# Performance work log

Measured on AMD Instinct MI355X. Metric: run time of the kernel, lower is better.

## Reference

```python
import jax, jax.numpy as jnp
import numpy as np

HIDDEN = 1024
INTER = 4096
EPS = 1e-12


def _ste(q, x):
    # straight-through estimator: forward q, backward identity wrt x
    return x + jax.lax.stop_gradient(q - x)


def setup_inputs() -> dict:
    key = jax.random.key(0)
    ks = jax.random.split(key, 4)
    hidden_states = jax.random.normal(ks[0], (4, 2048, INTER), dtype=jnp.float32)
    input_tensor = jax.random.normal(ks[1], (4, 2048, HIDDEN), dtype=jnp.float32)
    W = jax.random.normal(ks[2], (HIDDEN, INTER), dtype=jnp.float32) * 0.02
    b = jnp.zeros((HIDDEN,), dtype=jnp.float32)
    clip_val = jnp.asarray(2.5, dtype=jnp.float32)  # learnable elastic alpha
    gamma = jnp.ones((HIDDEN,), dtype=jnp.float32)
    beta = jnp.zeros((HIDDEN,), dtype=jnp.float32)
    return {"hidden_states": hidden_states, "input_tensor": input_tensor,
            "W": W, "b": b, "clip_val": clip_val, "gamma": gamma, "beta": beta}


def reference(hidden_states, input_tensor, W, b, clip_val, gamma, beta):
    # --- binary weight (BWN): per-output-channel scale = mean(|W|, axis=in) ---
    w_scale = jnp.mean(jnp.abs(W), axis=1, keepdims=True)  # [hidden, 1]
    W_q = _ste(w_scale * jnp.sign(W), W)                    # [hidden, inter]
    # --- elastic signed binary activation: q = alpha * sign(x / alpha) ---
    s = hidden_states / clip_val
    x_q = clip_val * _ste(jnp.sign(s), s)                   # [b, s, inter]
    # --- dense projection ---
    h = jnp.einsum('bsi,hi->bsh', x_q, W_q) + b             # [b, s, hidden]
    # dropout prob 0.0 (eval mode) -> no-op
    # --- residual + LayerNorm (eps=1e-12) ---
    r = h + input_tensor
    mu = jnp.mean(r, axis=-1, keepdims=True)
    var = jnp.mean(jnp.square(r - mu), axis=-1, keepdims=True)
    out = (r - mu) * jax.lax.rsqrt(var + EPS) * gamma + beta
    return out
```

## Files before the change

kernel.cpp:

```cpp
#include <hip/hip_runtime.h>
#include <stdint.h>

#define HIDDEN 1024
#define INTER  4096
#define ROWS   8192
#define BM     128
#define BN     128
#define NKSTEP 64
#define NBLK   512
#define BSTEP  65536

typedef int i32x4 __attribute__((ext_vector_type(4)));

__device__ __forceinline__ uint32_t sgn4(float4 v) {
    uint32_t b0 = (v.x < 0.f) ? 0xFFu : 0x01u;
    uint32_t b1 = (v.y < 0.f) ? 0xFFu : 0x01u;
    uint32_t b2 = (v.z < 0.f) ? 0xFFu : 0x01u;
    uint32_t b3 = (v.w < 0.f) ? 0xFFu : 0x01u;
    return b0 | (b1 << 8) | (b2 << 16) | (b3 << 24);
}

__global__ __launch_bounds__(256)
void pack_w_kernel(const float* __restrict__ W, uint8_t* __restrict__ Bg,
                   float* __restrict__ wscale) {
    int h = blockIdx.x;
    int tid = threadIdx.x;
    int lane = tid & 63, wv = tid >> 6;
    const float4* row = (const float4*)(W + (size_t)h * INTER);
    const uint32_t base_h = (uint32_t)(h >> 4) * 1024u + (uint32_t)(h & 15) * 16u;
    float asum = 0.f;
    #pragma unroll
    for (int q = 0; q < 4; ++q) {
        int g = q * 256 + tid;
        float4 v = row[g];
        asum += fabsf(v.x) + fabsf(v.y) + fabsf(v.z) + fabsf(v.w);
        uint32_t off = (uint32_t)(g >> 4) * (uint32_t)BSTEP + base_h
                     + (uint32_t)((g & 15) >> 2) * 256u + (uint32_t)(g & 3) * 4u;
        *(uint32_t*)(Bg + off) = sgn4(v);
    }
    #pragma unroll
    for (int off = 32; off > 0; off >>= 1) asum += __shfl_down(asum, off);
    __shared__ float red[4];
    if (lane == 0) red[wv] = asum;
    __syncthreads();
    if (tid == 0) wscale[h] = (red[0] + red[1] + red[2] + red[3]) * (1.0f / INTER);
}

__global__ __launch_bounds__(512, 4)
void gemm_kernel(const float* __restrict__ hs, const float* __restrict__ input,
                 const float* __restrict__ bias, const float* __restrict__ clipp,
                 float* __restrict__ out, const uint8_t* __restrict__ Bg,
                 const float* __restrict__ wscale) {
    __shared__ alignas(16) uint8_t sA[2 * 8192];

    const int tid  = threadIdx.x;
    const int lane = tid & 63;
    const int wave = tid >> 6;
    const int mt   = blockIdx.x & 63;
    const int ch   = blockIdx.x >> 6;
    const int m0   = mt * BM;

    const int r  = tid >> 2;
    const int kc = tid & 3;
    const int awofs = (r >> 4) * 1024 + (kc * 16 + (r & 15)) * 16;
    const float* aload = hs + (size_t)(m0 + r) * INTER + kc * 16;

    const uint8_t* bbase = Bg + (size_t)(ch * 8 + wave) * 1024 + lane * 16;
    const int fofs = lane * 16;

    i32x4 acc[8];
    #pragma unroll
    for (int rt = 0; rt < 8; ++rt) acc[rt] = (i32x4){0, 0, 0, 0};
    i32x4 Bb0, Bb1;
    float4 av0, av1, av2, av3;

    av0 = *(const float4*)(aload + 0);
    av1 = *(const float4*)(aload + 4);
    av2 = *(const float4*)(aload + 8);
    av3 = *(const float4*)(aload + 12);
    Bb0 = *(const i32x4*)(bbase);
    {
        i32x4 sg = (i32x4){(int)sgn4(av0), (int)sgn4(av1),
                           (int)sgn4(av2), (int)sgn4(av3)};
        *(i32x4*)&sA[awofs] = sg;
    }
    av0 = *(const float4*)(aload + 64);
    av1 = *(const float4*)(aload + 68);
    av2 = *(const float4*)(aload + 72);
    av3 = *(const float4*)(aload + 76);
    asm volatile("s_waitcnt lgkmcnt(0)" ::: "memory");
    __builtin_amdgcn_s_barrier();

#define BODY(T, CUR, BC, BN_, PFB, PFA) do {                                   \
    const uint8_t* ab_ = sA + (CUR) * 8192;                                    \
    i32x4 af0_ = *(const i32x4*)&ab_[0 * 1024 + fofs];                         \
    i32x4 af1_ = *(const i32x4*)&ab_[1 * 1024 + fofs];                         \
    i32x4 af2_ = *(const i32x4*)&ab_[2 * 1024 + fofs];                         \
    i32x4 af3_ = *(const i32x4*)&ab_[3 * 1024 + fofs];                         \
    i32x4 af4_ = *(const i32x4*)&ab_[4 * 1024 + fofs];                         \
    i32x4 af5_ = *(const i32x4*)&ab_[5 * 1024 + fofs];                         \
    i32x4 af6_ = *(const i32x4*)&ab_[6 * 1024 + fofs];                         \
    i32x4 af7_ = *(const i32x4*)&ab_[7 * 1024 + fofs];                         \
    if (PFB) Bb##BN_ = *(const i32x4*)(bbase + (size_t)((T) + 1) * BSTEP);     \
    __builtin_amdgcn_s_setprio(1);                                             \
    acc[0] = __builtin_amdgcn_mfma_i32_16x16x64_i8(af0_, Bb##BC, acc[0], 0, 0, 0); \
    acc[1] = __builtin_amdgcn_mfma_i32_16x16x64_i8(af1_, Bb##BC, acc[1], 0, 0, 0); \
    acc[2] = __builtin_amdgcn_mfma_i32_16x16x64_i8(af2_, Bb##BC, acc[2], 0, 0, 0); \
    acc[3] = __builtin_amdgcn_mfma_i32_16x16x64_i8(af3_, Bb##BC, acc[3], 0, 0, 0); \
    acc[4] = __builtin_amdgcn_mfma_i32_16x16x64_i8(af4_, Bb##BC, acc[4], 0, 0, 0); \
    acc[5] = __builtin_amdgcn_mfma_i32_16x16x64_i8(af5_, Bb##BC, acc[5], 0, 0, 0); \
    acc[6] = __builtin_amdgcn_mfma_i32_16x16x64_i8(af6_, Bb##BC, acc[6], 0, 0, 0); \
    acc[7] = __builtin_amdgcn_mfma_i32_16x16x64_i8(af7_, Bb##BC, acc[7], 0, 0, 0); \
    __builtin_amdgcn_s_setprio(0);                                             \
    if (PFB) {                                                                 \
        i32x4 sg_ = (i32x4){(int)sgn4(av0), (int)sgn4(av1),                    \
                            (int)sgn4(av2), (int)sgn4(av3)};                   \
        *(i32x4*)&sA[((CUR) ^ 1) * 8192 + awofs] = sg_;                        \
        if (PFA) {                                                             \
            av0 = *(const float4*)(aload + ((T) + 2) * 64 + 0);                \
            av1 = *(const float4*)(aload + ((T) + 2) * 64 + 4);                \
            av2 = *(const float4*)(aload + ((T) + 2) * 64 + 8);                \
            av3 = *(const float4*)(aload + ((T) + 2) * 64 + 12);               \
        }                                                                      \
        asm volatile("s_waitcnt lgkmcnt(0)" ::: "memory");                     \
        __builtin_amdgcn_s_barrier();                                          \
    }                                                                          \
} while (0)

    for (int tt = 0; tt < 31; ++tt) {
        BODY(2 * tt,     0, 0, 1, 1, 1);
        BODY(2 * tt + 1, 1, 1, 0, 1, 1);
    }
    BODY(62, 0, 0, 1, 1, 0);
    BODY(63, 1, 1, 0, 0, 0);
#undef BODY

    const float clip = clipp[0];
    const int l15 = lane & 15;
    const int gcol = ch * BN + wave * 16 + l15;
    const float cw = clip * wscale[gcol];
    const float bi = bias[gcol];
    const int rbase = (lane >> 4) * 4;
    #pragma unroll
    for (int rt = 0; rt < 8; ++rt) {
        #pragma unroll
        for (int rg = 0; rg < 4; ++rg) {
            size_t gidx = (size_t)(m0 + rt * 16 + rbase + rg) * HIDDEN + gcol;
            out[gidx] = fmaf((float)acc[rt][rg], cw, bi + input[gidx]);
        }
    }
}

__global__ __launch_bounds__(256)
void ln_kernel(float* __restrict__ out, const float* __restrict__ gamma,
               const float* __restrict__ beta) {
    const int lane = threadIdx.x & 63;
    const int wave = threadIdx.x >> 6;
    const int row  = blockIdx.x * 4 + wave;
    float4* rowp = (float4*)(out + (size_t)row * HIDDEN);
    const float4* gm4 = (const float4*)gamma;
    const float4* bt4 = (const float4*)beta;

    float4 v0 = rowp[lane +   0];
    float4 v1 = rowp[lane +  64];
    float4 v2 = rowp[lane + 128];
    float4 v3 = rowp[lane + 192];
    float s = v0.x + v0.y + v0.z + v0.w + v1.x + v1.y + v1.z + v1.w
            + v2.x + v2.y + v2.z + v2.w + v3.x + v3.y + v3.z + v3.w;
    float q = v0.x * v0.x + v0.y * v0.y + v0.z * v0.z + v0.w * v0.w
            + v1.x * v1.x + v1.y * v1.y + v1.z * v1.z + v1.w * v1.w
            + v2.x * v2.x + v2.y * v2.y + v2.z * v2.z + v2.w * v2.w
            + v3.x * v3.x + v3.y * v3.y + v3.z * v3.z + v3.w * v3.w;
    #pragma unroll
    for (int off = 1; off < 64; off <<= 1) {
        s += __shfl_xor(s, off);
        q += __shfl_xor(q, off);
    }
    float mu  = s * (1.0f / HIDDEN);
    float var = fmaf(-mu, mu, q * (1.0f / HIDDEN));
    float rs  = rsqrtf(var + 1e-12f);

    #pragma unroll
    for (int j = 0; j < 4; ++j) {
        int idx = lane + j * 64;
        float4 y = (j == 0) ? v0 : (j == 1) ? v1 : (j == 2) ? v2 : v3;
        float4 g = gm4[idx], b = bt4[idx];
        float4 o;
        o.x = (y.x - mu) * rs * g.x + b.x;
        o.y = (y.y - mu) * rs * g.y + b.y;
        o.z = (y.z - mu) * rs * g.z + b.z;
        o.w = (y.w - mu) * rs * g.w + b.w;
        rowp[idx] = o;
    }
}

extern "C" void kernel_launch(void* const* d_in, const int* in_sizes, int n_in,
                              void* d_out, int out_size, void* d_ws, size_t ws_size,
                              hipStream_t stream) {
    const float* hs    = (const float*)d_in[0];
    const float* inp   = (const float*)d_in[1];
    const float* W     = (const float*)d_in[2];
    const float* b     = (const float*)d_in[3];
    const float* clip  = (const float*)d_in[4];
    const float* gamma = (const float*)d_in[5];
    const float* beta  = (const float*)d_in[6];
    float* out = (float*)d_out;

    uint8_t* Bg   = (uint8_t*)d_ws;
    float* wscale = (float*)((char*)d_ws + 4u * 1024u * 1024u);

    pack_w_kernel<<<HIDDEN, 256, 0, stream>>>(W, Bg, wscale);
    gemm_kernel<<<NBLK, 512, 0, stream>>>(hs, inp, b, clip, out, Bg, wscale);
    ln_kernel<<<ROWS / 4, 256, 0, stream>>>(out, gamma, beta);
}
```

Before: 314.4 us.

## Pre-pack activation signs to int8 and use register-tiled GEMM without LDS

Adds a separate kernel that converts hidden_states to packed int8 signs in an MFMA-friendly layout in the workspace. The GEMM now loads both A and B fragments directly from global memory into registers, using a 2x2 wave grid with 4x4 MFMA tiles per wave, with no shared memory or barriers. Previously each 128x128 block re-read fp32 activations for every column chunk and converted them in-kernel. The change reduces fp32 traffic inside the GEMM but adds an extra pass that writes and reads 32 MB of int8 A, and relies on L2 for reuse of A across the 8 column tiles.

```diff
diff --git a/kernel.cpp b/kernel.cpp
--- a/kernel.cpp
+++ b/kernel.cpp
@@ -4,11 +4,9 @@
 #define HIDDEN 1024
 #define INTER  4096
 #define ROWS   8192
-#define BM     128
-#define BN     128
 #define NKSTEP 64
-#define NBLK   512
-#define BSTEP  65536
+#define B_KSTEP 65536
+#define A_KSTEP 524288
 
 typedef int i32x4 __attribute__((ext_vector_type(4)));
 
@@ -19,6 +17,7 @@
     uint32_t b3 = (v.w < 0.f) ? 0xFFu : 0x01u;
     return b0 | (b1 << 8) | (b2 << 16) | (b3 << 24);
 }
+
 
 __global__ __launch_bounds__(256)
 void pack_w_kernel(const float* __restrict__ W, uint8_t* __restrict__ Bg,
@@ -34,7 +33,7 @@
         int g = q * 256 + tid;
         float4 v = row[g];
         asum += fabsf(v.x) + fabsf(v.y) + fabsf(v.z) + fabsf(v.w);
-        uint32_t off = (uint32_t)(g >> 4) * (uint32_t)BSTEP + base_h
+        uint32_t off = (uint32_t)(g >> 4) * (uint32_t)B_KSTEP + base_h
                      + (uint32_t)((g & 15) >> 2) * 256u + (uint32_t)(g & 3) * 4u;
         *(uint32_t*)(Bg + off) = sgn4(v);
     }
@@ -46,107 +45,101 @@
     if (tid == 0) wscale[h] = (red[0] + red[1] + red[2] + red[3]) * (1.0f / INTER);
 }
 
-__global__ __launch_bounds__(512, 4)
-void gemm_kernel(const float* __restrict__ hs, const float* __restrict__ input,
-                 const float* __restrict__ bias, const float* __restrict__ clipp,
-                 float* __restrict__ out, const uint8_t* __restrict__ Bg,
+__global__ __launch_bounds__(256)
+void pack_a_kernel(const float* __restrict__ hs, uint8_t* __restrict__ Ag) {
+    int m = blockIdx.x;
+    int tid = threadIdx.x;
+    const float4* row = (const float4*)(hs + (size_t)m * INTER);
+    const uint32_t base_m = (uint32_t)(m >> 4) * 1024u + (uint32_t)(m & 15) * 16u;
+    #pragma unroll
+    for (int q = 0; q < 4; ++q) {
+        int g = q * 256 + tid;
+        float4 v = row[g];
+        uint32_t off = (uint32_t)(g >> 4) * (uint32_t)A_KSTEP + base_m
+                     + (uint32_t)((g & 15) >> 2) * 256u + (uint32_t)(g & 3) * 4u;
+        *(uint32_t*)(Ag + off) = sgn4(v);
+    }
+}
+
+__global__ __launch_bounds__(256, 3)
+void gemm_kernel(const float* __restrict__ input, const float* __restrict__ bias,
+                 const float* __restrict__ clipp, float* __restrict__ out,
+                 const uint8_t* __restrict__ Ag, const uint8_t* __restrict__ Bg,
                  const float* __restrict__ wscale) {
-    __shared__ alignas(16) uint8_t sA[2 * 8192];
-
     const int tid  = threadIdx.x;
     const int lane = tid & 63;
     const int wave = tid >> 6;
-    const int mt   = blockIdx.x & 63;
-    const int ch   = blockIdx.x >> 6;
-    const int m0   = mt * BM;
-
-    const int r  = tid >> 2;
-    const int kc = tid & 3;
-    const int awofs = (r >> 4) * 1024 + (kc * 16 + (r & 15)) * 16;
-    const float* aload = hs + (size_t)(m0 + r) * INTER + kc * 16;
-
-    const uint8_t* bbase = Bg + (size_t)(ch * 8 + wave) * 1024 + lane * 16;
-    const int fofs = lane * 16;
-
-    i32x4 acc[8];
-    #pragma unroll
-    for (int rt = 0; rt < 8; ++rt) acc[rt] = (i32x4){0, 0, 0, 0};
-    i32x4 Bb0, Bb1;
-    float4 av0, av1, av2, av3;
-
-    av0 = *(const float4*)(aload + 0);
-    av1 = *(const float4*)(aload + 4);
-    av2 = *(const float4*)(aload + 8);
-    av3 = *(const float4*)(aload + 12);
-    Bb0 = *(const i32x4*)(bbase);
-    {
-        i32x4 sg = (i32x4){(int)sgn4(av0), (int)sgn4(av1),
-                           (int)sgn4(av2), (int)sgn4(av3)};
-        *(i32x4*)&sA[awofs] = sg;
-    }
-    av0 = *(const float4*)(aload + 64);
-    av1 = *(const float4*)(aload + 68);
-    av2 = *(const float4*)(aload + 72);
-    av3 = *(const float4*)(aload + 76);
-    asm volatile("s_waitcnt lgkmcnt(0)" ::: "memory");
-    __builtin_amdgcn_s_barrier();
-
-#define BODY(T, CUR, BC, BN_, PFB, PFA) do {                                   \
-    const uint8_t* ab_ = sA + (CUR) * 8192;                                    \
-    i32x4 af0_ = *(const i32x4*)&ab_[0 * 1024 + fofs];                         \
-    i32x4 af1_ = *(const i32x4*)&ab_[1 * 1024 + fofs];                         \
-    i32x4 af2_ = *(const i32x4*)&ab_[2 * 1024 + fofs];                         \
-    i32x4 af3_ = *(const i32x4*)&ab_[3 * 1024 + fofs];                         \
-    i32x4 af4_ = *(const i32x4*)&ab_[4 * 1024 + fofs];                         \
-    i32x4 af5_ = *(const i32x4*)&ab_[5 * 1024 + fofs];                         \
-    i32x4 af6_ = *(const i32x4*)&ab_[6 * 1024 + fofs];                         \
-    i32x4 af7_ = *(const i32x4*)&ab_[7 * 1024 + fofs];                         \
-    if (PFB) Bb##BN_ = *(const i32x4*)(bbase + (size_t)((T) + 1) * BSTEP);     \
+    const int ct   = blockIdx.x & 7;
+    const int mt   = blockIdx.x >> 3;
+    const int wr   = wave >> 1, wc = wave & 1;
+    const int R0   = mt * 128 + wr * 64;
+    const int C0   = ct * 128 + wc * 64;
+
+    const uint8_t* aB = Ag + (size_t)(R0 >> 4) * 1024 + lane * 16;
+    const uint8_t* bB = Bg + (size_t)(C0 >> 4) * 1024 + lane * 16;
+
+    i32x4 acc[4][4];
+    #pragma unroll
+    for (int i = 0; i < 4; ++i)
+        #pragma unroll
+        for (int j = 0; j < 4; ++j) acc[i][j] = (i32x4){0, 0, 0, 0};
+
+    i32x4 Af0[4], Bf0[4], Af1[4], Bf1[4];
+
+    #pragma unroll
+    for (int u = 0; u < 4; ++u) {
+        Af0[u] = *(const i32x4*)(aB + u * 1024);
+        Bf0[u] = *(const i32x4*)(bB + u * 1024);
+    }
+
+#define STEP(T, BC, BN_, PF) do {                                              \
+    if (PF) {                                                                  \
+        const uint8_t* ap_ = aB + (size_t)((T) + 1) * A_KSTEP;                 \
+        const uint8_t* bp_ = bB + (size_t)((T) + 1) * B_KSTEP;                 \
+        _Pragma("unroll")                                                      \
+        for (int u_ = 0; u_ < 4; ++u_) {                                       \
+            Af##BN_[u_] = *(const i32x4*)(ap_ + u_ * 1024);                    \
+            Bf##BN_[u_] = *(const i32x4*)(bp_ + u_ * 1024);                    \
+        }                                                                      \
+    }                                                                          \
     __builtin_amdgcn_s_setprio(1);                                             \
-    acc[0] = __builtin_amdgcn_mfma_i32_16x16x64_i8(af0_, Bb##BC, acc[0], 0, 0, 0); \
-    acc[1] = __builtin_amdgcn_mfma_i32_16x16x64_i8(af1_, Bb##BC, acc[1], 0, 0, 0); \
-    acc[2] = __builtin_amdgcn_mfma_i32_16x16x64_i8(af2_, Bb##BC, acc[2], 0, 0, 0); \
-    acc[3] = __builtin_amdgcn_mfma_i32_16x16x64_i8(af3_, Bb##BC, acc[3], 0, 0, 0); \
-    acc[4] = __builtin_amdgcn_mfma_i32_16x16x64_i8(af4_, Bb##BC, acc[4], 0, 0, 0); \
-    acc[5] = __builtin_amdgcn_mfma_i32_16x16x64_i8(af5_, Bb##BC, acc[5], 0, 0, 0); \
-    acc[6] = __builtin_amdgcn_mfma_i32_16x16x64_i8(af6_, Bb##BC, acc[6], 0, 0, 0); \
-    acc[7] = __builtin_amdgcn_mfma_i32_16x16x64_i8(af7_, Bb##BC, acc[7], 0, 0, 0); \
+    _Pragma("unroll")                                                          \
+    for (int i_ = 0; i_ < 4; ++i_)                                             \
+        _Pragma("unroll")                                                      \
+        for (int j_ = 0; j_ < 4; ++j_)                                         \
+            acc[i_][j_] = __builtin_amdgcn_mfma_i32_16x16x64_i8(               \
+                Af##BC[i_], Bf##BC[j_], acc[i_][j_], 0, 0, 0);                 \
     __builtin_amdgcn_s_setprio(0);                                             \
-    if (PFB) {                                                                 \
-        i32x4 sg_ = (i32x4){(int)sgn4(av0), (int)sgn4(av1),                    \
-                            (int)sgn4(av2), (int)sgn4(av3)};                   \
-        *(i32x4*)&sA[((CUR) ^ 1) * 8192 + awofs] = sg_;                        \
-        if (PFA) {                                                             \
-            av0 = *(const float4*)(aload + ((T) + 2) * 64 + 0);                \
-            av1 = *(const float4*)(aload + ((T) + 2) * 64 + 4);                \
-            av2 = *(const float4*)(aload + ((T) + 2) * 64 + 8);                \
-            av3 = *(const float4*)(aload + ((T) + 2) * 64 + 12);               \
-        }                                                                      \
-        asm volatile("s_waitcnt lgkmcnt(0)" ::: "memory");                     \
-        __builtin_amdgcn_s_barrier();                                          \
-    }                                                                          \
 } while (0)
 
     for (int tt = 0; tt < 31; ++tt) {
-        BODY(2 * tt,     0, 0, 1, 1, 1);
-        BODY(2 * tt + 1, 1, 1, 0, 1, 1);
-    }
-    BODY(62, 0, 0, 1, 1, 0);
-    BODY(63, 1, 1, 0, 0, 0);
-#undef BODY
+        STEP(2 * tt,     0, 1, 1);
+        STEP(2 * tt + 1, 1, 0, 1);
+    }
+    STEP(62, 0, 1, 1);
+    STEP(63, 1, 0, 0);
+#undef STEP
 
     const float clip = clipp[0];
     const int l15 = lane & 15;
-    const int gcol = ch * BN + wave * 16 + l15;
-    const float cw = clip * wscale[gcol];
-    const float bi = bias[gcol];
-    const int rbase = (lane >> 4) * 4;
-    #pragma unroll
-    for (int rt = 0; rt < 8; ++rt) {
+    const int rb  = (lane >> 4) * 4;
+    float cw[4], bi[4];
+    #pragma unroll
+    for (int j = 0; j < 4; ++j) {
+        int gcol = C0 + j * 16 + l15;
+        cw[j] = clip * wscale[gcol];
+        bi[j] = bias[gcol];
+    }
+    #pragma unroll
+    for (int i = 0; i < 4; ++i) {
         #pragma unroll
         for (int rg = 0; rg < 4; ++rg) {
-            size_t gidx = (size_t)(m0 + rt * 16 + rbase + rg) * HIDDEN + gcol;
-            out[gidx] = fmaf((float)acc[rt][rg], cw, bi + input[gidx]);
+            int row = R0 + i * 16 + rb + rg;
+            #pragma unroll
+            for (int j = 0; j < 4; ++j) {
+                size_t gidx = (size_t)row * HIDDEN + C0 + j * 16 + l15;
+                out[gidx] = fmaf((float)acc[i][j][rg], cw[j], bi[j] + input[gidx]);
+            }
         }
     }
 }
@@ -207,9 +200,11 @@
     float* out = (float*)d_out;
 
     uint8_t* Bg   = (uint8_t*)d_ws;
-    float* wscale = (float*)((char*)d_ws + 4u * 1024u * 1024u);
+    uint8_t* Ag   = (uint8_t*)d_ws + (size_t)4 * 1024 * 1024;
+    float* wscale = (float*)((char*)d_ws + (size_t)36 * 1024 * 1024);
 
     pack_w_kernel<<<HIDDEN, 256, 0, stream>>>(W, Bg, wscale);
-    gemm_kernel<<<NBLK, 512, 0, stream>>>(hs, inp, b, clip, out, Bg, wscale);
+    pack_a_kernel<<<ROWS, 256, 0, stream>>>(hs, Ag);
+    gemm_kernel<<<512, 256, 0, stream>>>(inp, b, clip, out, Ag, Bg, wscale);
     ln_kernel<<<ROWS / 4, 256, 0, stream>>>(out, gamma, beta);
 }
```

New measurement: 324.8 us. 1.03x slower.
